# Kernel optimization log

Hardware: AMD Instinct MI355X
Metric: run time of the kernel (lower is better)

The kernel has to match this reference:

```python
import jax, jax.numpy as jnp
import numpy as np

# static config (matches init_kwargs)
STRIDE, PAD, DIL, DG = 1, 1, 1, 1
KH, KW = 3, 3
CIN, COUT = 64, 64


def setup_inputs() -> dict:
    key = jax.random.key(0)
    k1, k2, k3, k4 = jax.random.split(key, 4)
    N, C, H, W = 4, CIN, 128, 128
    K = KH * KW
    x = jax.random.normal(k1, (N, C, H, W), dtype=jnp.float32)
    offset = jax.random.normal(k2, (N, 2 * DG * K, H, W), dtype=jnp.float32)
    mask = jax.random.uniform(k3, (N, DG * K, H, W), dtype=jnp.float32)
    stdv = 1.0 / np.sqrt(C * K)
    weight = jax.random.uniform(k4, (COUT, C, KH, KW), dtype=jnp.float32,
                                minval=-stdv, maxval=stdv)
    bias = jnp.zeros((COUT,), dtype=jnp.float32)  # no_bias=True -> frozen zeros
    return {"x": x, "offset": offset, "mask": mask, "weight": weight, "bias": bias}


def _dcnv2(x, offset, mask, weight, bias):
    N, C, H, W = x.shape
    Cout, _, kh, kw = weight.shape
    K = kh * kw
    Ho = (H + 2 * PAD - DIL * (kh - 1) - 1) // STRIDE + 1
    Wo = (W + 2 * PAD - DIL * (kw - 1) - 1) // STRIDE + 1
    Cg = C // DG

    # offsets: [N, DG, K, 2(y,x), Ho, Wo]; mask: [N, DG, K, Ho, Wo]
    off = offset.reshape(N, DG, K, 2, Ho, Wo)
    off_y, off_x = off[:, :, :, 0], off[:, :, :, 1]
    m = mask.reshape(N, DG, K, Ho, Wo)

    kidx = jnp.arange(K)
    ky, kx = kidx // kw, kidx % kw
    base_y = (jnp.arange(Ho) * STRIDE - PAD)[None, :] + (ky * DIL)[:, None]  # [K,Ho]
    base_x = (jnp.arange(Wo) * STRIDE - PAD)[None, :] + (kx * DIL)[:, None]  # [K,Wo]

    py = base_y[None, None, :, :, None].astype(x.dtype) + off_y  # [N,DG,K,Ho,Wo]
    px = base_x[None, None, :, None, :].astype(x.dtype) + off_x

    y0 = jnp.floor(py)
    x0 = jnp.floor(px)
    ly = py - y0  # frac weights
    lx = px - x0
    y0i = y0.astype(jnp.int32)
    x0i = x0.astype(jnp.int32)

    xf = x.reshape(N, DG, Cg, H * W)

    def gather(yi, xi):
        # per-corner zero padding (out-of-bounds corners contribute 0)
        valid = ((yi >= 0) & (yi < H) & (xi >= 0) & (xi < W))
        idx = jnp.clip(yi, 0, H - 1) * W + jnp.clip(xi, 0, W - 1)  # [N,DG,K,Ho,Wo]
        idx_b = jnp.broadcast_to(idx[:, :, None], (N, DG, Cg, K, Ho, Wo))
        v = jnp.take_along_axis(xf, idx_b.reshape(N, DG, Cg, -1), axis=3)
        v = v.reshape(N, DG, Cg, K, Ho, Wo)
        return v * valid[:, :, None].astype(x.dtype)

    w00 = ((1 - ly) * (1 - lx))[:, :, None]  # [N,DG,1,K,Ho,Wo]
    w01 = ((1 - ly) * lx)[:, :, None]
    w10 = (ly * (1 - lx))[:, :, None]
    w11 = (ly * lx)[:, :, None]

    val = (gather(y0i, x0i) * w00 + gather(y0i, x0i + 1) * w01
           + gather(y0i + 1, x0i) * w10 + gather(y0i + 1, x0i + 1) * w11)
    cols = val * m[:, :, None]                      # modulation
    cols = cols.reshape(N, C, K, Ho, Wo)            # DG*Cg -> C (contiguous)

    wmat = weight.reshape(Cout, C, K)
    out = jnp.einsum('nckhw,ock->nohw', cols, wmat)
    return out + bias[None, :, None, None]


def reference(x, offset, mask, weight, bias):
    return _dcnv2(x, offset, mask, weight, bias)
```

## Files before the change

kernel.cpp:

```cpp
#include <hip/hip_runtime.h>

#define N_    4
#define C_    64
#define H_    128
#define W_    128
#define KW_   3
#define K_    9
#define COUT_ 64
#define HW_   (H_ * W_)
#define NPIX  (N_ * HW_)
#define KK_   (C_ * K_)

typedef short v8s __attribute__((ext_vector_type(8)));
typedef float v4f __attribute__((ext_vector_type(4)));
typedef int   v4i __attribute__((ext_vector_type(4)));
typedef unsigned int u32;
typedef unsigned short u16;
typedef unsigned int v2u __attribute__((ext_vector_type(2)));

static __device__ __forceinline__ u16 f2bf(float f) {
    union { float f; unsigned int u; } v; v.f = f;
    unsigned int r = v.u + 0x7FFFu + ((v.u >> 16) & 1u);
    return (u16)(r >> 16);
}
static __device__ __forceinline__ u32 pack2(float lo, float hi) {
    return ((u32)f2bf(hi) << 16) | (u32)f2bf(lo);
}

__global__ __launch_bounds__(256) void prep(
    const float* __restrict__ x, float* __restrict__ xh,
    const float* __restrict__ w, u16* __restrict__ wA3)
{
    if (blockIdx.x < 1024) {
        const int n   = blockIdx.x >> 8;
        const int hw0 = (blockIdx.x & 255) * 64;
        const int j   = threadIdx.x & 63;
        const int r0  = threadIdx.x >> 6;

        __shared__ float tile[64][65];
        const float* xb = x + n * (C_ * HW_);
#pragma unroll
        for (int i = 0; i < 16; ++i) {
            const int c = i * 4 + r0;
            tile[j][c] = xb[c * HW_ + hw0 + j];
        }
        __syncthreads();
        float* xo = xh + ((size_t)n * HW_ + hw0) * 64;
#pragma unroll
        for (int i = 0; i < 16; ++i) {
            const int hr = i * 4 + r0;
            xo[hr * 64 + j] = tile[hr][j];
        }
    } else {
        const int tid = (blockIdx.x - 1024) * 256 + threadIdx.x;
        if (tid < COUT_ * KK_) {
            const int k   = tid % KK_;
            const int o   = tid / KK_;
            const int c   = k & 63;
            const int tap = k >> 6;
            wA3[tid] = f2bf(w[o * (C_ * K_) + c * K_ + tap]);
        }
    }
}

__global__ __launch_bounds__(256, 4) void dcn_fused(
    const float* __restrict__ xh,
    const float* __restrict__ offset,
    const float* __restrict__ mask,
    const u16* __restrict__ wA3,
    const float* __restrict__ bias,
    float* __restrict__ out)
{
    const int tid  = threadIdx.x;
    const int lane = tid & 63;
    const int wv   = tid >> 6;
    const int quad = lane >> 4;
    const int l16  = lane & 15;

    const int lb  = (blockIdx.x & 7) * 128 + (blockIdx.x >> 3);
    const int pxb = lb * 64;
    const int n   = pxb >> 14;
    const int hwb = pxb & (HW_ - 1);

    __shared__ float coef[576][8];
    __shared__ u16   Bt[2][64][72];

#pragma unroll
    for (int r = 0; r < 3; ++r) {
        const int e = tid + 256 * r;
        if (e < 576) {
            const int p  = e / 9;
            const int t  = e - p * 9;
            const int hw = hwb + p;
            const int ho = hw >> 7;
            const int wo = hw & (W_ - 1);
            const int ky = t / KW_;
            const int kx = t - ky * KW_;

            const float offy = offset[n * (2 * K_ * HW_) + (2 * t + 0) * HW_ + hw];
            const float offx = offset[n * (2 * K_ * HW_) + (2 * t + 1) * HW_ + hw];
            const float mval = mask[n * (K_ * HW_) + t * HW_ + hw];

            const float py = (float)(ho - 1 + ky) + offy;
            const float qx = (float)(wo - 1 + kx) + offx;
            const float y0f = floorf(py), x0f = floorf(qx);
            const float ly = py - y0f, lx = qx - x0f;
            const int y0 = (int)y0f, x0 = (int)x0f;
            const int y1 = y0 + 1,   x1 = x0 + 1;
            const bool vy0 = (y0 >= 0) & (y0 < H_);
            const bool vy1 = (y1 >= 0) & (y1 < H_);
            const bool vx0 = (x0 >= 0) & (x0 < W_);
            const bool vx1 = (x1 >= 0) & (x1 < W_);
            const int cy0 = min(max(y0, 0), H_ - 1);
            const int cy1 = min(max(y1, 0), H_ - 1);
            const int cx0 = min(max(x0, 0), W_ - 1);
            const int cx1 = min(max(x1, 0), W_ - 1);

            float* q = &coef[e][0];
            q[0] = (1.f - ly) * (1.f - lx) * mval * ((vy0 && vx0) ? 1.f : 0.f);
            q[1] = (1.f - ly) * lx         * mval * ((vy0 && vx1) ? 1.f : 0.f);
            q[2] = ly         * (1.f - lx) * mval * ((vy1 && vx0) ? 1.f : 0.f);
            q[3] = ly         * lx         * mval * ((vy1 && vx1) ? 1.f : 0.f);
            int* qi = (int*)q;
            qi[4] = cy0 * W_ + cx0;
            qi[5] = cy0 * W_ + cx1;
            qi[6] = cy1 * W_ + cx0;
            qi[7] = cy1 * W_ + cx1;
        }
    }
    __syncthreads();

    const int qtr = lane >> 4;
    const int c4  = lane & 15;
    const float* xb4 = xh + ((size_t)n * HW_) * 64 + 4 * c4;

    const int mb   = (wv & 1) * 32;
    const int pxwl = (wv >> 1) * 32;

    v4f acc[2][2];
#pragma unroll
    for (int mh = 0; mh < 2; ++mh)
#pragma unroll
        for (int nh = 0; nh < 2; ++nh)
            acc[mh][nh] = (v4f){0.f, 0.f, 0.f, 0.f};

#define GATHER(t, b)                                                        \
    {                                                                       \
        _Pragma("unroll")                                                   \
        for (int i = 0; i < 4; ++i) {                                       \
            const int p = wv * 16 + 4 * i + qtr;                            \
            const float* q = &coef[p * 9 + (t)][0];                         \
            const v4f f = *(const v4f*)q;                                   \
            const v4i o = *(const v4i*)(q + 4);                             \
            const v4f v00 = *(const v4f*)(xb4 + (size_t)o.x * 64);          \
            const v4f v01 = *(const v4f*)(xb4 + (size_t)o.y * 64);          \
            const v4f v10 = *(const v4f*)(xb4 + (size_t)o.z * 64);          \
            const v4f v11 = *(const v4f*)(xb4 + (size_t)o.w * 64);          \
            float r0 = fmaf(f.x, v00.x, fmaf(f.y, v01.x,                    \
                       fmaf(f.z, v10.x, f.w * v11.x)));                     \
            float r1 = fmaf(f.x, v00.y, fmaf(f.y, v01.y,                    \
                       fmaf(f.z, v10.y, f.w * v11.y)));                     \
            float r2 = fmaf(f.x, v00.z, fmaf(f.y, v01.z,                    \
                       fmaf(f.z, v10.z, f.w * v11.z)));                     \
            float r3 = fmaf(f.x, v00.w, fmaf(f.y, v01.w,                    \
                       fmaf(f.z, v10.w, f.w * v11.w)));                     \
            v2u pk;                                                         \
            pk.x = pack2(r0, r1);                                           \
            pk.y = pack2(r2, r3);                                           \
            *(v2u*)&Bt[b][p][4 * c4] = pk;                                  \
        }                                                                   \
    }

    GATHER(0, 0)
    __syncthreads();

    for (int t = 0; t < K_; ++t) {
        const int buf = t & 1;
        if (t < K_ - 1) GATHER(t + 1, buf ^ 1)

#pragma unroll
        for (int kc = 0; kc < 2; ++kc) {
            v8s bfr[2];
#pragma unroll
            for (int nh = 0; nh < 2; ++nh)
                bfr[nh] = *(const v8s*)&Bt[buf][pxwl + nh * 16 + l16][kc * 32 + quad * 8];
            v8s afr[2];
#pragma unroll
            for (int mh = 0; mh < 2; ++mh)
                afr[mh] = *(const v8s*)(wA3 + (size_t)(mb + mh * 16 + l16) * KK_
                                            + t * 64 + kc * 32 + quad * 8);
#pragma unroll
            for (int mh = 0; mh < 2; ++mh)
#pragma unroll
                for (int nh = 0; nh < 2; ++nh)
                    acc[mh][nh] = __builtin_amdgcn_mfma_f32_16x16x32_bf16(
                        afr[mh], bfr[nh], acc[mh][nh], 0, 0, 0);
        }
        __syncthreads();
    }
#undef GATHER

    float* outb = out + n * (COUT_ * HW_);
#pragma unroll
    for (int mh = 0; mh < 2; ++mh)
#pragma unroll
        for (int nh = 0; nh < 2; ++nh)
#pragma unroll
            for (int r = 0; r < 4; ++r) {
                const int m = mb + mh * 16 + quad * 4 + r;
                outb[m * HW_ + hwb + pxwl + nh * 16 + l16] = acc[mh][nh][r] + bias[m];
            }
}

__global__ __launch_bounds__(256) void dcn_fallback(
    const float* __restrict__ x, const float* __restrict__ offset,
    const float* __restrict__ mask, const float* __restrict__ wptr,
    const float* __restrict__ bias, float* __restrict__ out)
{
    const int pix = blockIdx.x * 256 + threadIdx.x;
    const int n = pix >> 14, hw = pix & (HW_ - 1);
    const int ho = hw >> 7,  wo = hw & (W_ - 1);
    float acc[COUT_];
#pragma unroll
    for (int o = 0; o < COUT_; ++o) acc[o] = bias[o];
    const float* xn   = x + n * (C_ * HW_);
    const float* offn = offset + n * (2 * K_ * HW_) + hw;
    const float* mn   = mask + n * (K_ * HW_) + hw;
    for (int ct = 0; ct < C_; ct += 8) {
        for (int k = 0; k < K_; ++k) {
            const int ky = k / KW_, kx = k - ky * KW_;
            const float off_y = offn[(2 * k + 0) * HW_];
            const float off_x = offn[(2 * k + 1) * HW_];
            const float m = mn[k * HW_];
            const float py = (float)(ho - 1 + ky) + off_y;
            const float px = (float)(wo - 1 + kx) + off_x;
            const float y0f = floorf(py), x0f = floorf(px);
            const float ly = py - y0f, lx = px - x0f;
            const int y0 = (int)y0f, x0 = (int)x0f, y1 = y0 + 1, x1 = x0 + 1;
            const bool vy0 = (y0 >= 0) & (y0 < H_), vy1 = (y1 >= 0) & (y1 < H_);
            const bool vx0 = (x0 >= 0) & (x0 < W_), vx1 = (x1 >= 0) & (x1 < W_);
            const int cy0 = min(max(y0, 0), H_ - 1), cy1 = min(max(y1, 0), H_ - 1);
            const int cx0 = min(max(x0, 0), W_ - 1), cx1 = min(max(x1, 0), W_ - 1);
            const int i00 = cy0 * W_ + cx0, i01 = cy0 * W_ + cx1;
            const int i10 = cy1 * W_ + cx0, i11 = cy1 * W_ + cx1;
            const float f00 = (1.f - ly) * (1.f - lx) * m * ((vy0 && vx0) ? 1.f : 0.f);
            const float f01 = (1.f - ly) * lx * m * ((vy0 && vx1) ? 1.f : 0.f);
            const float f10 = ly * (1.f - lx) * m * ((vy1 && vx0) ? 1.f : 0.f);
            const float f11 = ly * lx * m * ((vy1 && vx1) ? 1.f : 0.f);
            for (int cc = 0; cc < 8; ++cc) {
                const int c = ct + cc;
                const float* xc = xn + c * HW_;
                const float val = fmaf(f00, xc[i00], fmaf(f01, xc[i01],
                                  fmaf(f10, xc[i10], f11 * xc[i11])));
#pragma unroll
                for (int o = 0; o < COUT_; ++o)
                    acc[o] = fmaf(wptr[o * (C_ * K_) + c * K_ + k], val, acc[o]);
            }
        }
    }
    float* outp = out + n * (COUT_ * HW_) + hw;
#pragma unroll
    for (int o = 0; o < COUT_; ++o) outp[o * HW_] = acc[o];
}

extern "C" void kernel_launch(void* const* d_in, const int* in_sizes, int n_in,
                              void* d_out, int out_size, void* d_ws, size_t ws_size,
                              hipStream_t stream) {
    const float* x      = (const float*)d_in[0];
    const float* offset = (const float*)d_in[1];
    const float* mask   = (const float*)d_in[2];
    const float* weight = (const float*)d_in[3];
    const float* bias   = (const float*)d_in[4];
    float* out = (float*)d_out;

    const size_t xh_bytes = (size_t)NPIX * C_ * sizeof(float);
    const size_t wA_bytes = (size_t)COUT_ * KK_ * sizeof(u16);

    if (ws_size >= xh_bytes + wA_bytes) {
        float* xh  = (float*)d_ws;
        u16*   wA3 = (u16*)((char*)d_ws + xh_bytes);
        prep<<<1024 + 144, 256, 0, stream>>>(x, xh, weight, wA3);
        dcn_fused<<<NPIX / 64, 256, 0, stream>>>(xh, offset, mask, wA3, bias, out);
    } else {
        dcn_fallback<<<NPIX / 256, 256, 0, stream>>>(x, offset, mask, weight, bias, out);
    }
}
```

Baseline: 122.7 us.

## Gather MFMA B fragments directly into registers, dropping LDS staging and barriers

The fused kernel now has each wave gather and bilinearly blend the input values for its own 16 pixels straight into the MFMA B-operand registers. This removes the double-buffered LDS tile and the per-tap __syncthreads. Each wave computes all 64 output channels for its pixels, so the weight fragments are read four times per tap instead of two. The change also uses the hardware v_cvt_pk_bf16_f32 instruction for bf16 packing, vectorizes the prep transpose with float4 loads and stores, and lowers launch_bounds occupancy from 4 to 2 to make room for more registers. The trade-off is higher register pressure and lower occupancy in exchange for no LDS round-trip and no block-level synchronization.

```diff
diff --git a/kernel.cpp b/kernel.cpp
--- a/kernel.cpp
+++ b/kernel.cpp
@@ -16,15 +16,16 @@
 typedef int   v4i __attribute__((ext_vector_type(4)));
 typedef unsigned int u32;
 typedef unsigned short u16;
-typedef unsigned int v2u __attribute__((ext_vector_type(2)));
 
 static __device__ __forceinline__ u16 f2bf(float f) {
     union { float f; unsigned int u; } v; v.f = f;
     unsigned int r = v.u + 0x7FFFu + ((v.u >> 16) & 1u);
     return (u16)(r >> 16);
 }
-static __device__ __forceinline__ u32 pack2(float lo, float hi) {
-    return ((u32)f2bf(hi) << 16) | (u32)f2bf(lo);
+static __device__ __forceinline__ u32 cvtpk(float lo, float hi) {
+    u32 r;
+    asm("v_cvt_pk_bf16_f32 %0, %1, %2" : "=v"(r) : "v"(lo), "v"(hi));
+    return r;
 }
 
 __global__ __launch_bounds__(256) void prep(
@@ -34,22 +35,33 @@
     if (blockIdx.x < 1024) {
         const int n   = blockIdx.x >> 8;
         const int hw0 = (blockIdx.x & 255) * 64;
-        const int j   = threadIdx.x & 63;
-        const int r0  = threadIdx.x >> 6;
 
         __shared__ float tile[64][65];
         const float* xb = x + n * (C_ * HW_);
 #pragma unroll
-        for (int i = 0; i < 16; ++i) {
-            const int c = i * 4 + r0;
-            tile[j][c] = xb[c * HW_ + hw0 + j];
+        for (int i = 0; i < 4; ++i) {
+            const int idx = i * 256 + threadIdx.x;
+            const int q   = idx & 15;
+            const int c   = idx >> 4;
+            const v4f v = *(const v4f*)&xb[c * HW_ + hw0 + 4 * q];
+            tile[4 * q + 0][c] = v.x;
+            tile[4 * q + 1][c] = v.y;
+            tile[4 * q + 2][c] = v.z;
+            tile[4 * q + 3][c] = v.w;
         }
         __syncthreads();
         float* xo = xh + ((size_t)n * HW_ + hw0) * 64;
 #pragma unroll
-        for (int i = 0; i < 16; ++i) {
-            const int hr = i * 4 + r0;
-            xo[hr * 64 + j] = tile[hr][j];
+        for (int i = 0; i < 4; ++i) {
+            const int idx = i * 256 + threadIdx.x;
+            const int c4  = idx & 15;
+            const int hr  = idx >> 4;
+            v4f v;
+            v.x = tile[hr][4 * c4 + 0];
+            v.y = tile[hr][4 * c4 + 1];
+            v.z = tile[hr][4 * c4 + 2];
+            v.w = tile[hr][4 * c4 + 3];
+            *(v4f*)&xo[hr * 64 + 4 * c4] = v;
         }
     } else {
         const int tid = (blockIdx.x - 1024) * 256 + threadIdx.x;
@@ -63,7 +75,7 @@
     }
 }
 
-__global__ __launch_bounds__(256, 4) void dcn_fused(
+__global__ __launch_bounds__(256, 2) void dcn_fused(
     const float* __restrict__ xh,
     const float* __restrict__ offset,
     const float* __restrict__ mask,
@@ -82,8 +94,8 @@
     const int n   = pxb >> 14;
     const int hwb = pxb & (HW_ - 1);
 
-    __shared__ float coef[576][8];
-    __shared__ u16   Bt[2][64][72];
+    __shared__ float cw[576][4];
+    __shared__ int   ci[576][4];
 
 #pragma unroll
     for (int r = 0; r < 3; ++r) {
@@ -116,100 +128,79 @@
             const int cx0 = min(max(x0, 0), W_ - 1);
             const int cx1 = min(max(x1, 0), W_ - 1);
 
-            float* q = &coef[e][0];
+            float* q = &cw[e][0];
             q[0] = (1.f - ly) * (1.f - lx) * mval * ((vy0 && vx0) ? 1.f : 0.f);
             q[1] = (1.f - ly) * lx         * mval * ((vy0 && vx1) ? 1.f : 0.f);
             q[2] = ly         * (1.f - lx) * mval * ((vy1 && vx0) ? 1.f : 0.f);
             q[3] = ly         * lx         * mval * ((vy1 && vx1) ? 1.f : 0.f);
-            int* qi = (int*)q;
-            qi[4] = cy0 * W_ + cx0;
-            qi[5] = cy0 * W_ + cx1;
-            qi[6] = cy1 * W_ + cx0;
-            qi[7] = cy1 * W_ + cx1;
+            int* qi = &ci[e][0];
+            qi[0] = cy0 * W_ + cx0;
+            qi[1] = cy0 * W_ + cx1;
+            qi[2] = cy1 * W_ + cx0;
+            qi[3] = cy1 * W_ + cx1;
         }
     }
     __syncthreads();
 
-    const int qtr = lane >> 4;
-    const int c4  = lane & 15;
-    const float* xb4 = xh + ((size_t)n * HW_) * 64 + 4 * c4;
-
-    const int mb   = (wv & 1) * 32;
-    const int pxwl = (wv >> 1) * 32;
-
-    v4f acc[2][2];
-#pragma unroll
-    for (int mh = 0; mh < 2; ++mh)
-#pragma unroll
-        for (int nh = 0; nh < 2; ++nh)
-            acc[mh][nh] = (v4f){0.f, 0.f, 0.f, 0.f};
-
-#define GATHER(t, b)                                                        \
-    {                                                                       \
-        _Pragma("unroll")                                                   \
-        for (int i = 0; i < 4; ++i) {                                       \
-            const int p = wv * 16 + 4 * i + qtr;                            \
-            const float* q = &coef[p * 9 + (t)][0];                         \
-            const v4f f = *(const v4f*)q;                                   \
-            const v4i o = *(const v4i*)(q + 4);                             \
-            const v4f v00 = *(const v4f*)(xb4 + (size_t)o.x * 64);          \
-            const v4f v01 = *(const v4f*)(xb4 + (size_t)o.y * 64);          \
-            const v4f v10 = *(const v4f*)(xb4 + (size_t)o.z * 64);          \
-            const v4f v11 = *(const v4f*)(xb4 + (size_t)o.w * 64);          \
-            float r0 = fmaf(f.x, v00.x, fmaf(f.y, v01.x,                    \
-                       fmaf(f.z, v10.x, f.w * v11.x)));                     \
-            float r1 = fmaf(f.x, v00.y, fmaf(f.y, v01.y,                    \
-                       fmaf(f.z, v10.y, f.w * v11.y)));                     \
-            float r2 = fmaf(f.x, v00.z, fmaf(f.y, v01.z,                    \
-                       fmaf(f.z, v10.z, f.w * v11.z)));                     \
-            float r3 = fmaf(f.x, v00.w, fmaf(f.y, v01.w,                    \
-                       fmaf(f.z, v10.w, f.w * v11.w)));                     \
-            v2u pk;                                                         \
-            pk.x = pack2(r0, r1);                                           \
-            pk.y = pack2(r2, r3);                                           \
-            *(v2u*)&Bt[b][p][4 * c4] = pk;                                  \
-        }                                                                   \
-    }
-
-    GATHER(0, 0)
-    __syncthreads();
-
+    const int pxw = wv * 16;
+    const int pxl = pxw + l16;
+    const float* xb = xh + ((size_t)n * HW_) * 64 + quad * 8;
+
+    v4f acc[4];
+#pragma unroll
+    for (int mh = 0; mh < 4; ++mh) acc[mh] = (v4f){0.f, 0.f, 0.f, 0.f};
+
+#pragma unroll
     for (int t = 0; t < K_; ++t) {
-        const int buf = t & 1;
-        if (t < K_ - 1) GATHER(t + 1, buf ^ 1)
+        const v4f f = *(const v4f*)&cw[pxl * 9 + t][0];
+        const v4i o = *(const v4i*)&ci[pxl * 9 + t][0];
+        const float* p0 = xb + (size_t)o.x * 64;
+        const float* p1 = xb + (size_t)o.y * 64;
+        const float* p2 = xb + (size_t)o.z * 64;
+        const float* p3 = xb + (size_t)o.w * 64;
+        v4f c0[4], c1[4], c2[4], c3[4];
+        c0[0] = *(const v4f*)(p0);      c0[1] = *(const v4f*)(p0 + 4);
+        c0[2] = *(const v4f*)(p0 + 32); c0[3] = *(const v4f*)(p0 + 36);
+        c1[0] = *(const v4f*)(p1);      c1[1] = *(const v4f*)(p1 + 4);
+        c1[2] = *(const v4f*)(p1 + 32); c1[3] = *(const v4f*)(p1 + 36);
+        c2[0] = *(const v4f*)(p2);      c2[1] = *(const v4f*)(p2 + 4);
+        c2[2] = *(const v4f*)(p2 + 32); c2[3] = *(const v4f*)(p2 + 36);
+        c3[0] = *(const v4f*)(p3);      c3[1] = *(const v4f*)(p3 + 4);
+        c3[2] = *(const v4f*)(p3 + 32); c3[3] = *(const v4f*)(p3 + 36);
+
+        float rr[16];
+#pragma unroll
+        for (int h = 0; h < 4; ++h)
+#pragma unroll
+            for (int j = 0; j < 4; ++j)
+                rr[h * 4 + j] = fmaf(f.x, c0[h][j], fmaf(f.y, c1[h][j],
+                                fmaf(f.z, c2[h][j], f.w * c3[h][j])));
+
+        union { v8s v[2]; u32 w[8]; } B;
+#pragma unroll
+        for (int i = 0; i < 8; ++i)
+            B.w[i] = cvtpk(rr[2 * i], rr[2 * i + 1]);
 
 #pragma unroll
         for (int kc = 0; kc < 2; ++kc) {
-            v8s bfr[2];
-#pragma unroll
-            for (int nh = 0; nh < 2; ++nh)
-                bfr[nh] = *(const v8s*)&Bt[buf][pxwl + nh * 16 + l16][kc * 32 + quad * 8];
-            v8s afr[2];
-#pragma unroll
-            for (int mh = 0; mh < 2; ++mh)
-                afr[mh] = *(const v8s*)(wA3 + (size_t)(mb + mh * 16 + l16) * KK_
-                                            + t * 64 + kc * 32 + quad * 8);
-#pragma unroll
-            for (int mh = 0; mh < 2; ++mh)
-#pragma unroll
-                for (int nh = 0; nh < 2; ++nh)
-                    acc[mh][nh] = __builtin_amdgcn_mfma_f32_16x16x32_bf16(
-                        afr[mh], bfr[nh], acc[mh][nh], 0, 0, 0);
-        }
-        __syncthreads();
-    }
-#undef GATHER
-
-    float* outb = out + n * (COUT_ * HW_);
-#pragma unroll
-    for (int mh = 0; mh < 2; ++mh)
-#pragma unroll
-        for (int nh = 0; nh < 2; ++nh)
-#pragma unroll
-            for (int r = 0; r < 4; ++r) {
-                const int m = mb + mh * 16 + quad * 4 + r;
-                outb[m * HW_ + hwb + pxwl + nh * 16 + l16] = acc[mh][nh][r] + bias[m];
+            const u16* ap = wA3 + (size_t)l16 * KK_ + t * 64 + kc * 32 + quad * 8;
+#pragma unroll
+            for (int mh = 0; mh < 4; ++mh) {
+                const v8s afr = *(const v8s*)(ap + (size_t)mh * 16 * KK_);
+                acc[mh] = __builtin_amdgcn_mfma_f32_16x16x32_bf16(
+                    afr, B.v[kc], acc[mh], 0, 0, 0);
             }
+        }
+    }
+
+    float* outb = out + n * (COUT_ * HW_) + hwb + pxw + l16;
+#pragma unroll
+    for (int mh = 0; mh < 4; ++mh)
+#pragma unroll
+        for (int r = 0; r < 4; ++r) {
+            const int m = mh * 16 + quad * 4 + r;
+            outb[m * HW_] = acc[mh][r] + bias[m];
+        }
 }
 
 __global__ __launch_bounds__(256) void dcn_fallback(
```

New measurement: 175.4 us. 42.9% more time.
